# Performance work log

Hardware: AMD Instinct MI355X
Metric: run time of the kernel (lower is better)

Reference implementation:

```python
import jax, jax.numpy as jnp
import numpy as np

NUM_HEADS = 16
HEAD_DIM = 64  # hidden_size 1024 / 16 heads


def setup_inputs() -> dict:
    key = jax.random.key(0)
    ks = jax.random.split(key, 5)
    B, S, D = 4, 2048, 1024
    std = 0.02
    return {
        "hidden_states": jax.random.normal(ks[0], (B, S, D), jnp.float32),
        "attention_mask": jnp.zeros((B, 1, 1, S), jnp.float32),
        "Wq": jax.random.normal(ks[1], (D, D), jnp.float32) * std,
        "bq": jnp.zeros((D,), jnp.float32),
        "Wk": jax.random.normal(ks[2], (D, D), jnp.float32) * std,
        "bk": jnp.zeros((D,), jnp.float32),
        "Wv": jax.random.normal(ks[3], (D, D), jnp.float32) * std,
        "bv": jnp.zeros((D,), jnp.float32),
    }


def _split_heads(x):
    # [B, S, H*dh] -> [B, H, S, dh]
    B, S, _ = x.shape
    return x.reshape(B, S, NUM_HEADS, HEAD_DIM).transpose(0, 2, 1, 3)


def reference(hidden_states, attention_mask, Wq, bq, Wk, bk, Wv, bv):
    q = _split_heads(hidden_states @ Wq + bq)  # [B,H,S,dh]
    k = _split_heads(hidden_states @ Wk + bk)
    v = _split_heads(hidden_states @ Wv + bv)
    scale = 1.0 / jnp.sqrt(jnp.asarray(HEAD_DIM, q.dtype))
    scores = jnp.einsum("bhqd,bhkd->bhqk", q, k) * scale
    scores = scores + attention_mask.astype(scores.dtype)
    probs = jax.nn.softmax(scores, axis=-1)  # dropout prob = 0 -> identity
    ctx = jnp.einsum("bhqk,bhkd->bhqd", probs, v)
    B, H, S, dh = ctx.shape
    return ctx.transpose(0, 2, 1, 3).reshape(B, S, H * dh)
```

## Files before the change

### kernel.cpp

```cpp
#include <hip/hip_runtime.h>
#include <stdint.h>

typedef unsigned short u16;
typedef __attribute__((ext_vector_type(4))) float f32x4;
typedef __attribute__((ext_vector_type(8))) short bf16x8;
typedef __attribute__((ext_vector_type(4))) int i32x4;

#define LOG2E 1.4426950408889634f

__device__ inline u16 f2b(float x) {
  union { float f; uint32_t u; } t; t.f = x;
  uint32_t r = t.u + 0x7FFFu + ((t.u >> 16) & 1u);
  return (u16)(r >> 16);
}

__device__ inline int cvtpk(float a, float b) {
  int r;
  asm("v_cvt_pk_bf16_f32 %0, %1, %2" : "=v"(r) : "v"(a), "v"(b));
  return r;
}

__device__ inline float exp2a(float x) {
  float r;
  asm("v_exp_f32 %0, %1" : "=v"(r) : "v"(x));
  return r;
}

typedef const __attribute__((address_space(1))) void* gas_t;
typedef __attribute__((address_space(3))) void* las_t;
__device__ inline void gld16(const void* g, void* l) {
  __builtin_amdgcn_global_load_lds((gas_t)g, (las_t)l, 16, 0, 0);
}

__global__ void cvt_hs_k(const float* __restrict__ in, u16* __restrict__ outp, int n) {
  int i = (blockIdx.x * 256 + threadIdx.x) * 4;
  if (i >= n) return;
  float4 v = *(const float4*)(in + i);
  ushort4 o = { f2b(v.x), f2b(v.y), f2b(v.z), f2b(v.w) };
  *(ushort4*)(outp + i) = o;
}

__global__ void twk(const float* __restrict__ Wq, const float* __restrict__ Wk,
                    const float* __restrict__ Wv, u16* __restrict__ Wt) {
  __shared__ float tile[64][65];
  const float* W = (blockIdx.z == 0) ? Wq : ((blockIdx.z == 1) ? Wk : Wv);
  int n0 = blockIdx.x * 64, k0 = blockIdx.y * 64;
  int tid = threadIdx.x;
#pragma unroll 4
  for (int i = 0; i < 16; ++i) {
    int idx = i * 256 + tid; int r = idx >> 6, c = idx & 63;
    tile[r][c] = W[(k0 + r) * 1024 + n0 + c];
  }
  __syncthreads();
  u16* dst = Wt + blockIdx.z * 1048576;
#pragma unroll 4
  for (int i = 0; i < 16; ++i) {
    int idx = i * 256 + tid; int r = idx >> 6, c = idx & 63;
    dst[(n0 + r) * 1024 + k0 + c] = f2b(tile[c][r]);
  }
}

__global__ __launch_bounds__(256) void qkv_gemm_k(
    const u16* __restrict__ hsb, const u16* __restrict__ wt,
    const float* __restrict__ bq, const float* __restrict__ bk, const float* __restrict__ bv,
    u16* __restrict__ Qo, u16* __restrict__ Ko, u16* __restrict__ Vto) {
  __shared__ u16 t1[128 * 64];
  __shared__ u16 t2[128 * 64];
  const int tid = threadIdx.x;
  const int w = tid >> 6, l = tid & 63, g = l >> 4, lm = l & 15;

  int lin = blockIdx.y * 24 + blockIdx.x;
  lin = (lin & 7) * 192 + (lin >> 3);
  const int bx = lin % 24, by = lin / 24;

  const int nbase = bx * 128;
  const int wi = nbase >> 10;
  const int nloc0 = nbase & 1023;
  const int mbase = by * 128;
  const bool swapped = (wi < 2);
  const u16* T1g = swapped ? (wt + wi * 1048576 + nloc0 * 1024) : (hsb + mbase * 1024);
  const u16* T2g = swapped ? (hsb + mbase * 1024) : (wt + 2 * 1048576 + nloc0 * 1024);

  f32x4 acc[4][4];
#pragma unroll
  for (int i = 0; i < 4; ++i)
#pragma unroll
    for (int j = 0; j < 4; ++j)
#pragma unroll
      for (int r = 0; r < 4; ++r) acc[i][j][r] = 0.f;

  const int r1w = (w >> 1) * 64;
  const int r2w = (w & 1) * 64;

  for (int kb = 0; kb < 1024; kb += 64) {
    __syncthreads();
#pragma unroll
    for (int p = 0; p < 4; ++p) {
      int idx = p * 256 + tid;
      int r = idx >> 3, c = idx & 7;
      int sc = (c ^ (r & 7)) << 3;
      gld16(T1g + r * 1024 + kb + sc, t1 + idx * 8);
      gld16(T2g + r * 1024 + kb + sc, t2 + idx * 8);
    }
    __syncthreads();
#pragma unroll
    for (int ks = 0; ks < 2; ++ks) {
      bf16x8 fa[4], fb[4];
#pragma unroll
      for (int i = 0; i < 4; ++i) {
        int ra = r1w + i * 16 + lm;
        fa[i] = *(const bf16x8*)(t1 + ra * 64 + (((g + 4 * ks) ^ (ra & 7)) << 3));
        int rb = r2w + i * 16 + lm;
        fb[i] = *(const bf16x8*)(t2 + rb * 64 + (((g + 4 * ks) ^ (rb & 7)) << 3));
      }
      __builtin_amdgcn_s_setprio(1);
#pragma unroll
      for (int i = 0; i < 4; ++i)
#pragma unroll
        for (int j = 0; j < 4; ++j)
          acc[i][j] = __builtin_amdgcn_mfma_f32_16x16x32_bf16(fa[i], fb[j], acc[i][j], 0, 0, 0);
      __builtin_amdgcn_s_setprio(0);
    }
  }

  if (swapped) {
    u16* O = (wi == 0) ? Qo : Ko;
    const float* bias = (wi == 0) ? bq : bk;
#pragma unroll
    for (int i = 0; i < 4; ++i) {
      int nl = nloc0 + r1w + i * 16 + g * 4;
      f32x4 bv4 = *(const f32x4*)(bias + nl);
      int d = nl & 63, h = nl >> 6;
#pragma unroll
      for (int j = 0; j < 4; ++j) {
        int m = mbase + r2w + j * 16 + lm;
        int bb = m >> 11, s = m & 2047;
        f32x4 v = acc[i][j];
        ushort4 o = { f2b(v[0] + bv4[0]), f2b(v[1] + bv4[1]),
                      f2b(v[2] + bv4[2]), f2b(v[3] + bv4[3]) };
        *(ushort4*)(O + ((size_t)(bb * 16 + h) * 2048 + s) * 64 + d) = o;
      }
    }
  } else {
#pragma unroll
    for (int j = 0; j < 4; ++j) {
      int nl = nloc0 + r2w + j * 16 + lm;
      float bias = bv[nl];
      int d = nl & 63, h = nl >> 6;
#pragma unroll
      for (int i = 0; i < 4; ++i) {
        int m = mbase + r1w + i * 16 + g * 4;
        int bb = m >> 11, s = m & 2047;
        int cp = (s & ~31) | (((s >> 2) & 3) << 3) | (((s >> 4) & 1) << 2);
        f32x4 v = acc[i][j];
        ushort4 o = { f2b(v[0] + bias), f2b(v[1] + bias),
                      f2b(v[2] + bias), f2b(v[3] + bias) };
        *(ushort4*)(Vto + ((size_t)(bb * 16 + h) * 64 + d) * 2048 + cp) = o;
      }
    }
  }
}

__global__ __launch_bounds__(512) void attn_k(
    const u16* __restrict__ Qg, const u16* __restrict__ Kg, const u16* __restrict__ Vtg,
    const float* __restrict__ maskg, float* __restrict__ outp) {
  __shared__ u16 kt[128 * 64];
  __shared__ u16 vt[64 * 128];
  __shared__ float mk[128];
  const int tid = threadIdx.x;
  const int w = tid >> 6, l = tid & 63, g = l >> 4, lm = l & 15;

  int bid = blockIdx.y * 16 + blockIdx.x;
  bid = (bid & 7) * 128 + (bid >> 3);
  const int bx = bid & 15, bh = bid >> 4;
  const int b = bh >> 4, h = bh & 15;
  const int q0 = bx * 128 + w * 16;
  const u16* Qb = Qg + ((size_t)bh * 2048 + q0) * 64;
  const u16* Kb = Kg + (size_t)bh * 2048 * 64;
  const u16* Vb = Vtg + (size_t)bh * 64 * 2048;
  const float* mb = maskg + b * 2048;

  bf16x8 qf0 = *(const bf16x8*)(Qb + lm * 64 + g * 8);
  bf16x8 qf1 = *(const bf16x8*)(Qb + lm * 64 + 32 + g * 8);

  f32x4 ctx[4];
#pragma unroll
  for (int dt = 0; dt < 4; ++dt)
#pragma unroll
    for (int r = 0; r < 4; ++r) ctx[dt][r] = 0.f;
  float mrun = -3.0e38f, lrun = 0.f;
  const float QS = 0.125f * LOG2E;

  for (int kv = 0; kv < 2048; kv += 128) {
    __syncthreads();
#pragma unroll
    for (int p = 0; p < 2; ++p) {
      int idx = p * 512 + tid;
      int rk = idx >> 3, ck = idx & 7;
      gld16(Kb + (size_t)(kv + rk) * 64 + ((ck ^ (rk & 7)) << 3), kt + idx * 8);
      int rv = idx >> 4, cv = idx & 15;
      gld16(Vb + (size_t)rv * 2048 + kv + ((cv ^ (rv & 7)) << 3), vt + idx * 8);
    }
    if (tid < 128) mk[tid] = mb[kv + tid] * LOG2E;
    __syncthreads();

    f32x4 st[8];
#pragma unroll
    for (int t = 0; t < 8; ++t)
#pragma unroll
      for (int r = 0; r < 4; ++r) st[t][r] = 0.f;

    __builtin_amdgcn_s_setprio(1);
#pragma unroll
    for (int ks = 0; ks < 2; ++ks) {
      bf16x8 qf = ks ? qf1 : qf0;
#pragma unroll
      for (int t = 0; t < 8; ++t) {
        int r = t * 16 + lm;
        bf16x8 kf = *(const bf16x8*)(kt + r * 64 + (((g + 4 * ks) ^ (r & 7)) << 3));
        st[t] = __builtin_amdgcn_mfma_f32_16x16x32_bf16(kf, qf, st[t], 0, 0, 0);
      }
    }
    __builtin_amdgcn_s_setprio(0);

    float tmax = -3.0e38f;
#pragma unroll
    for (int t = 0; t < 8; ++t) {
      f32x4 mv = *(const f32x4*)(mk + t * 16 + g * 4);
#pragma unroll
      for (int r = 0; r < 4; ++r) st[t][r] = fmaf(st[t][r], QS, mv[r]);
      tmax = fmaxf(tmax, fmaxf(fmaxf(st[t][0], st[t][1]), fmaxf(st[t][2], st[t][3])));
    }
    tmax = fmaxf(tmax, __shfl_xor(tmax, 16));
    tmax = fmaxf(tmax, __shfl_xor(tmax, 32));

    if (!__all(tmax <= mrun + 8.0f)) {
      float mnew = fmaxf(mrun, tmax);
      float corr = exp2a(mrun - mnew);
      lrun *= corr;
#pragma unroll
      for (int dt = 0; dt < 4; ++dt)
#pragma unroll
        for (int r = 0; r < 4; ++r) ctx[dt][r] *= corr;
      mrun = mnew;
    }

    int pt[8][2];
    float lsum = 0.f;
#pragma unroll
    for (int t = 0; t < 8; ++t) {
      float p0 = exp2a(st[t][0] - mrun);
      float p1 = exp2a(st[t][1] - mrun);
      float p2 = exp2a(st[t][2] - mrun);
      float p3 = exp2a(st[t][3] - mrun);
      lsum += (p0 + p1) + (p2 + p3);
      pt[t][0] = cvtpk(p0, p1);
      pt[t][1] = cvtpk(p2, p3);
    }
    lsum += __shfl_xor(lsum, 16);
    lsum += __shfl_xor(lsum, 32);
    lrun += lsum;

    __builtin_amdgcn_s_setprio(1);
#pragma unroll
    for (int tp = 0; tp < 4; ++tp) {
      i32x4 pbi = { pt[2 * tp][0], pt[2 * tp][1], pt[2 * tp + 1][0], pt[2 * tp + 1][1] };
      bf16x8 pb = __builtin_bit_cast(bf16x8, pbi);
#pragma unroll
      for (int dt = 0; dt < 4; ++dt) {
        int r = dt * 16 + lm;
        bf16x8 va = *(const bf16x8*)(vt + r * 128 + (((tp * 4 + g) ^ (r & 7)) << 3));
        ctx[dt] = __builtin_amdgcn_mfma_f32_16x16x32_bf16(va, pb, ctx[dt], 0, 0, 0);
      }
    }
    __builtin_amdgcn_s_setprio(0);
  }

  float inv = 1.f / lrun;
  int sq = q0 + lm;
  float* ob = outp + ((size_t)(b * 2048 + sq)) * 1024 + h * 64;
#pragma unroll
  for (int dt = 0; dt < 4; ++dt) {
    f32x4 o;
#pragma unroll
    for (int r = 0; r < 4; ++r) o[r] = ctx[dt][r] * inv;
    *(f32x4*)(ob + dt * 16 + g * 4) = o;
  }
}

extern "C" void kernel_launch(void* const* d_in, const int* in_sizes, int n_in,
                              void* d_out, int out_size, void* d_ws, size_t ws_size,
                              hipStream_t stream) {
  const float* hs   = (const float*)d_in[0];
  const float* mask = (const float*)d_in[1];
  const float* Wq   = (const float*)d_in[2];
  const float* bq   = (const float*)d_in[3];
  const float* Wk   = (const float*)d_in[4];
  const float* bk   = (const float*)d_in[5];
  const float* Wv   = (const float*)d_in[6];
  const float* bv   = (const float*)d_in[7];
  float* out = (float*)d_out;

  char* ws = (char*)d_ws;
  u16* hsb = (u16*)(ws);
  u16* wt  = (u16*)(ws + (16u << 20));
  u16* Qb  = (u16*)(ws + (24u << 20));
  u16* Kb  = (u16*)(ws + (40u << 20));
  u16* Vtb = (u16*)(ws + (56u << 20));

  cvt_hs_k<<<dim3(8192), dim3(256), 0, stream>>>(hs, hsb, 8388608);
  twk<<<dim3(16, 16, 3), dim3(256), 0, stream>>>(Wq, Wk, Wv, wt);
  qkv_gemm_k<<<dim3(24, 64), dim3(256), 0, stream>>>(hsb, wt, bq, bk, bv, Qb, Kb, Vtb);
  attn_k<<<dim3(16, 64), dim3(512), 0, stream>>>(Qb, Kb, Vtb, mask, out);
}
```

Baseline: 267.6 us.

## Double-buffer LDS tiles in QKV GEMM and attention, enlarge GEMM tiles

The QKV GEMM moves to 256x256 tiles with 512 threads and double-buffered LDS, prefetching the next K slice while MFMAs run on the current one. The attention kernel also double-buffers its K/V tiles, preloads the whole mask row into LDS once, and uses a single vmcnt-wait barrier per iteration instead of two syncthreads. The aim is to hide global-load latency and cut barrier overhead. The cost is much higher LDS use (128KB in the GEMM, about 72KB in attention) and more register pressure, which may reduce occupancy.

```diff
diff --git a/kernel.cpp b/kernel.cpp
--- a/kernel.cpp
+++ b/kernel.cpp
@@ -30,6 +30,13 @@
 typedef __attribute__((address_space(3))) void* las_t;
 __device__ inline void gld16(const void* g, void* l) {
   __builtin_amdgcn_global_load_lds((gas_t)g, (las_t)l, 16, 0, 0);
+}
+
+__device__ inline void vm0_bar() {
+  asm volatile("s_waitcnt vmcnt(0)" ::: "memory");
+  __builtin_amdgcn_sched_barrier(0);
+  __builtin_amdgcn_s_barrier();
+  __builtin_amdgcn_sched_barrier(0);
 }
 
 __global__ void cvt_hs_k(const float* __restrict__ in, u16* __restrict__ outp, int n) {
@@ -60,101 +67,134 @@
   }
 }
 
-__global__ __launch_bounds__(256) void qkv_gemm_k(
+__global__ __launch_bounds__(512, 2) void qkv_gemm_k(
     const u16* __restrict__ hsb, const u16* __restrict__ wt,
     const float* __restrict__ bq, const float* __restrict__ bk, const float* __restrict__ bv,
     u16* __restrict__ Qo, u16* __restrict__ Ko, u16* __restrict__ Vto) {
-  __shared__ u16 t1[128 * 64];
-  __shared__ u16 t2[128 * 64];
+  __shared__ u16 lh[2][256 * 64];
+  __shared__ u16 lw[2][256 * 64];
   const int tid = threadIdx.x;
   const int w = tid >> 6, l = tid & 63, g = l >> 4, lm = l & 15;
-
-  int lin = blockIdx.y * 24 + blockIdx.x;
-  lin = (lin & 7) * 192 + (lin >> 3);
-  const int bx = lin % 24, by = lin / 24;
-
-  const int nbase = bx * 128;
+  const int wm = w >> 2, wn = w & 3;
+
+  int lin = blockIdx.y * 12 + blockIdx.x;
+  lin = (lin & 7) * 48 + (lin >> 3);
+  const int bx = lin % 12, by = lin / 12;
+  const int nbase = bx << 8;
   const int wi = nbase >> 10;
   const int nloc0 = nbase & 1023;
-  const int mbase = by * 128;
-  const bool swapped = (wi < 2);
-  const u16* T1g = swapped ? (wt + wi * 1048576 + nloc0 * 1024) : (hsb + mbase * 1024);
-  const u16* T2g = swapped ? (hsb + mbase * 1024) : (wt + 2 * 1048576 + nloc0 * 1024);
-
-  f32x4 acc[4][4];
-#pragma unroll
-  for (int i = 0; i < 4; ++i)
+  const int mbase = by << 8;
+  const u16* hsg = hsb + (size_t)mbase * 1024;
+  const u16* wg  = wt + (size_t)wi * 1048576 + (size_t)nloc0 * 1024;
+
+  f32x4 acc[8][4];
+#pragma unroll
+  for (int i = 0; i < 8; ++i)
 #pragma unroll
     for (int j = 0; j < 4; ++j)
 #pragma unroll
       for (int r = 0; r < 4; ++r) acc[i][j][r] = 0.f;
 
-  const int r1w = (w >> 1) * 64;
-  const int r2w = (w & 1) * 64;
-
-  for (int kb = 0; kb < 1024; kb += 64) {
-    __syncthreads();
-#pragma unroll
-    for (int p = 0; p < 4; ++p) {
-      int idx = p * 256 + tid;
-      int r = idx >> 3, c = idx & 7;
-      int sc = (c ^ (r & 7)) << 3;
-      gld16(T1g + r * 1024 + kb + sc, t1 + idx * 8);
-      gld16(T2g + r * 1024 + kb + sc, t2 + idx * 8);
-    }
-    __syncthreads();
-#pragma unroll
-    for (int ks = 0; ks < 2; ++ks) {
-      bf16x8 fa[4], fb[4];
-#pragma unroll
-      for (int i = 0; i < 4; ++i) {
-        int ra = r1w + i * 16 + lm;
-        fa[i] = *(const bf16x8*)(t1 + ra * 64 + (((g + 4 * ks) ^ (ra & 7)) << 3));
-        int rb = r2w + i * 16 + lm;
-        fb[i] = *(const bf16x8*)(t2 + rb * 64 + (((g + 4 * ks) ^ (rb & 7)) << 3));
+#pragma unroll
+  for (int p = 0; p < 4; ++p) {
+    int idx = p * 512 + tid;
+    int r = idx >> 3, c8 = idx & 7;
+    int sc = (c8 ^ (r & 7)) << 3;
+    gld16(hsg + (size_t)r * 1024 + sc, &lh[0][idx * 8]);
+    gld16(wg + (size_t)r * 1024 + sc, &lw[0][idx * 8]);
+  }
+  vm0_bar();
+
+  for (int t = 0; t < 16; ++t) {
+    const int cur = t & 1;
+    if (t < 15) {
+      const int kb = (t + 1) << 6;
+#pragma unroll
+      for (int p = 0; p < 4; ++p) {
+        int idx = p * 512 + tid;
+        int r = idx >> 3, c8 = idx & 7;
+        int sc = (c8 ^ (r & 7)) << 3;
+        gld16(hsg + (size_t)r * 1024 + kb + sc, &lh[cur ^ 1][idx * 8]);
+        gld16(wg + (size_t)r * 1024 + kb + sc, &lw[cur ^ 1][idx * 8]);
+      }
+    }
+    const u16* LH = lh[cur];
+    const u16* LW = lw[cur];
+    bf16x8 fw[4][2];
+#pragma unroll
+    for (int ni = 0; ni < 4; ++ni) {
+      int rb = wn * 64 + ni * 16 + lm;
+#pragma unroll
+      for (int ks = 0; ks < 2; ++ks)
+        fw[ni][ks] = *(const bf16x8*)(LW + rb * 64 + (((g + 4 * ks) ^ (rb & 7)) << 3));
+    }
+#pragma unroll
+    for (int mh = 0; mh < 2; ++mh) {
+      bf16x8 fh[4][2];
+#pragma unroll
+      for (int mi = 0; mi < 4; ++mi) {
+        int ra = wm * 128 + mh * 64 + mi * 16 + lm;
+#pragma unroll
+        for (int ks = 0; ks < 2; ++ks)
+          fh[mi][ks] = *(const bf16x8*)(LH + ra * 64 + (((g + 4 * ks) ^ (ra & 7)) << 3));
       }
       __builtin_amdgcn_s_setprio(1);
-#pragma unroll
-      for (int i = 0; i < 4; ++i)
-#pragma unroll
-        for (int j = 0; j < 4; ++j)
-          acc[i][j] = __builtin_amdgcn_mfma_f32_16x16x32_bf16(fa[i], fb[j], acc[i][j], 0, 0, 0);
+      if (wi < 2) {
+#pragma unroll
+        for (int mi = 0; mi < 4; ++mi)
+#pragma unroll
+          for (int ni = 0; ni < 4; ++ni)
+#pragma unroll
+            for (int ks = 0; ks < 2; ++ks)
+              acc[mh * 4 + mi][ni] = __builtin_amdgcn_mfma_f32_16x16x32_bf16(
+                  fw[ni][ks], fh[mi][ks], acc[mh * 4 + mi][ni], 0, 0, 0);
+      } else {
+#pragma unroll
+        for (int mi = 0; mi < 4; ++mi)
+#pragma unroll
+          for (int ni = 0; ni < 4; ++ni)
+#pragma unroll
+            for (int ks = 0; ks < 2; ++ks)
+              acc[mh * 4 + mi][ni] = __builtin_amdgcn_mfma_f32_16x16x32_bf16(
+                  fh[mi][ks], fw[ni][ks], acc[mh * 4 + mi][ni], 0, 0, 0);
+      }
       __builtin_amdgcn_s_setprio(0);
     }
-  }
-
-  if (swapped) {
+    vm0_bar();
+  }
+
+  if (wi < 2) {
     u16* O = (wi == 0) ? Qo : Ko;
     const float* bias = (wi == 0) ? bq : bk;
 #pragma unroll
-    for (int i = 0; i < 4; ++i) {
-      int nl = nloc0 + r1w + i * 16 + g * 4;
-      f32x4 bv4 = *(const f32x4*)(bias + nl);
+    for (int ni = 0; ni < 4; ++ni) {
+      int nl = nloc0 + wn * 64 + ni * 16 + g * 4;
+      f32x4 b4 = *(const f32x4*)(bias + nl);
       int d = nl & 63, h = nl >> 6;
 #pragma unroll
-      for (int j = 0; j < 4; ++j) {
-        int m = mbase + r2w + j * 16 + lm;
+      for (int mi = 0; mi < 8; ++mi) {
+        int m = mbase + wm * 128 + mi * 16 + lm;
         int bb = m >> 11, s = m & 2047;
-        f32x4 v = acc[i][j];
-        ushort4 o = { f2b(v[0] + bv4[0]), f2b(v[1] + bv4[1]),
-                      f2b(v[2] + bv4[2]), f2b(v[3] + bv4[3]) };
+        f32x4 v = acc[mi][ni];
+        ushort4 o = { f2b(v[0] + b4[0]), f2b(v[1] + b4[1]),
+                      f2b(v[2] + b4[2]), f2b(v[3] + b4[3]) };
         *(ushort4*)(O + ((size_t)(bb * 16 + h) * 2048 + s) * 64 + d) = o;
       }
     }
   } else {
 #pragma unroll
-    for (int j = 0; j < 4; ++j) {
-      int nl = nloc0 + r2w + j * 16 + lm;
-      float bias = bv[nl];
+    for (int ni = 0; ni < 4; ++ni) {
+      int nl = nloc0 + wn * 64 + ni * 16 + lm;
+      float bsc = bv[nl];
       int d = nl & 63, h = nl >> 6;
 #pragma unroll
-      for (int i = 0; i < 4; ++i) {
-        int m = mbase + r1w + i * 16 + g * 4;
+      for (int mi = 0; mi < 8; ++mi) {
+        int m = mbase + wm * 128 + mi * 16 + g * 4;
         int bb = m >> 11, s = m & 2047;
         int cp = (s & ~31) | (((s >> 2) & 3) << 3) | (((s >> 4) & 1) << 2);
-        f32x4 v = acc[i][j];
-        ushort4 o = { f2b(v[0] + bias), f2b(v[1] + bias),
-                      f2b(v[2] + bias), f2b(v[3] + bias) };
+        f32x4 v = acc[mi][ni];
+        ushort4 o = { f2b(v[0] + bsc), f2b(v[1] + bsc),
+                      f2b(v[2] + bsc), f2b(v[3] + bsc) };
         *(ushort4*)(Vto + ((size_t)(bb * 16 + h) * 64 + d) * 2048 + cp) = o;
       }
     }
@@ -164,9 +204,9 @@
 __global__ __launch_bounds__(512) void attn_k(
     const u16* __restrict__ Qg, const u16* __restrict__ Kg, const u16* __restrict__ Vtg,
     const float* __restrict__ maskg, float* __restrict__ outp) {
-  __shared__ u16 kt[128 * 64];
-  __shared__ u16 vt[64 * 128];
-  __shared__ float mk[128];
+  __shared__ u16 kts[2][128 * 64];
+  __shared__ u16 vts[2][64 * 128];
+  __shared__ float ml[2048];
   const int tid = threadIdx.x;
   const int w = tid >> 6, l = tid & 63, g = l >> 4, lm = l & 15;
 
@@ -191,45 +231,65 @@
   float mrun = -3.0e38f, lrun = 0.f;
   const float QS = 0.125f * LOG2E;
 
-  for (int kv = 0; kv < 2048; kv += 128) {
-    __syncthreads();
-#pragma unroll
-    for (int p = 0; p < 2; ++p) {
-      int idx = p * 512 + tid;
-      int rk = idx >> 3, ck = idx & 7;
-      gld16(Kb + (size_t)(kv + rk) * 64 + ((ck ^ (rk & 7)) << 3), kt + idx * 8);
-      int rv = idx >> 4, cv = idx & 15;
-      gld16(Vb + (size_t)rv * 2048 + kv + ((cv ^ (rv & 7)) << 3), vt + idx * 8);
-    }
-    if (tid < 128) mk[tid] = mb[kv + tid] * LOG2E;
-    __syncthreads();
+  {
+    f32x4 mv = *(const f32x4*)(mb + tid * 4);
+    *(f32x4*)(ml + tid * 4) = mv * LOG2E;
+  }
+#pragma unroll
+  for (int p = 0; p < 2; ++p) {
+    int idx = p * 512 + tid;
+    int rk = idx >> 3, ck = idx & 7;
+    gld16(Kb + (size_t)rk * 64 + ((ck ^ (rk & 7)) << 3), &kts[0][idx * 8]);
+    int rv = idx >> 4, cv = idx & 15;
+    gld16(Vb + (size_t)rv * 2048 + ((cv ^ (rv & 7)) << 3), &vts[0][idx * 8]);
+  }
+  asm volatile("s_waitcnt vmcnt(0) lgkmcnt(0)" ::: "memory");
+  __builtin_amdgcn_sched_barrier(0);
+  __builtin_amdgcn_s_barrier();
+  __builtin_amdgcn_sched_barrier(0);
+
+  for (int t = 0; t < 16; ++t) {
+    const int kv = t << 7, cur = t & 1;
+    if (t < 15) {
+      const int kv2 = kv + 128;
+#pragma unroll
+      for (int p = 0; p < 2; ++p) {
+        int idx = p * 512 + tid;
+        int rk = idx >> 3, ck = idx & 7;
+        gld16(Kb + (size_t)(kv2 + rk) * 64 + ((ck ^ (rk & 7)) << 3), &kts[cur ^ 1][idx * 8]);
+        int rv = idx >> 4, cv = idx & 15;
+        gld16(Vb + (size_t)rv * 2048 + kv2 + ((cv ^ (rv & 7)) << 3), &vts[cur ^ 1][idx * 8]);
+      }
+    }
+    const u16* kt = kts[cur];
+    const u16* vt = vts[cur];
 
     f32x4 st[8];
 #pragma unroll
-    for (int t = 0; t < 8; ++t)
-#pragma unroll
-      for (int r = 0; r < 4; ++r) st[t][r] = 0.f;
+    for (int t8 = 0; t8 < 8; ++t8)
+#pragma unroll
+      for (int r = 0; r < 4; ++r) st[t8][r] = 0.f;
 
     __builtin_amdgcn_s_setprio(1);
 #pragma unroll
     for (int ks = 0; ks < 2; ++ks) {
       bf16x8 qf = ks ? qf1 : qf0;
 #pragma unroll
-      for (int t = 0; t < 8; ++t) {
-        int r = t * 16 + lm;
+      for (int t8 = 0; t8 < 8; ++t8) {
+        int r = t8 * 16 + lm;
         bf16x8 kf = *(const bf16x8*)(kt + r * 64 + (((g + 4 * ks) ^ (r & 7)) << 3));
-        st[t] = __builtin_amdgcn_mfma_f32_16x16x32_bf16(kf, qf, st[t], 0, 0, 0);
+        st[t8] = __builtin_amdgcn_mfma_f32_16x16x32_bf16(kf, qf, st[t8], 0, 0, 0);
       }
     }
     __builtin_amdgcn_s_setprio(0);
 
     float tmax = -3.0e38f;
 #pragma unroll
-    for (int t = 0; t < 8; ++t) {
-      f32x4 mv = *(const f32x4*)(mk + t * 16 + g * 4);
-#pragma unroll
-      for (int r = 0; r < 4; ++r) st[t][r] = fmaf(st[t][r], QS, mv[r]);
-      tmax = fmaxf(tmax, fmaxf(fmaxf(st[t][0], st[t][1]), fmaxf(st[t][2], st[t][3])));
+    for (int t8 = 0; t8 < 8; ++t8) {
+      f32x4 mv = *(const f32x4*)(ml + kv + t8 * 16 + g * 4);
+#pragma unroll
+      for (int r = 0; r < 4; ++r) st[t8][r] = fmaf(st[t8][r], QS, mv[r]);
+      tmax = fmaxf(fmaxf(fmaxf(fmaxf(st[t8][0], st[t8][1]), st[t8][2]), st[t8][3]), tmax);
     }
     tmax = fmaxf(tmax, __shfl_xor(tmax, 16));
     tmax = fmaxf(tmax, __shfl_xor(tmax, 32));
@@ -248,14 +308,14 @@
     int pt[8][2];
     float lsum = 0.f;
 #pragma unroll
-    for (int t = 0; t < 8; ++t) {
-      float p0 = exp2a(st[t][0] - mrun);
-      float p1 = exp2a(st[t][1] - mrun);
-      float p2 = exp2a(st[t][2] - mrun);
-      float p3 = exp2a(st[t][3] - mrun);
+    for (int t8 = 0; t8 < 8; ++t8) {
+      float p0 = exp2a(st[t8][0] - mrun);
+      float p1 = exp2a(st[t8][1] - mrun);
+      float p2 = exp2a(st[t8][2] - mrun);
+      float p3 = exp2a(st[t8][3] - mrun);
       lsum += (p0 + p1) + (p2 + p3);
-      pt[t][0] = cvtpk(p0, p1);
-      pt[t][1] = cvtpk(p2, p3);
+      pt[t8][0] = cvtpk(p0, p1);
+      pt[t8][1] = cvtpk(p2, p3);
     }
     lsum += __shfl_xor(lsum, 16);
     lsum += __shfl_xor(lsum, 32);
@@ -274,6 +334,8 @@
       }
     }
     __builtin_amdgcn_s_setprio(0);
+
+    vm0_bar();
   }
 
   float inv = 1.f / lrun;
@@ -310,6 +372,6 @@
 
   cvt_hs_k<<<dim3(8192), dim3(256), 0, stream>>>(hs, hsb, 8388608);
   twk<<<dim3(16, 16, 3), dim3(256), 0, stream>>>(Wq, Wk, Wv, wt);
-  qkv_gemm_k<<<dim3(24, 64), dim3(256), 0, stream>>>(hsb, wt, bq, bk, bv, Qb, Kb, Vtb);
+  qkv_gemm_k<<<dim3(12, 32), dim3(512), 0, stream>>>(hsb, wt, bq, bk, bv, Qb, Kb, Vtb);
   attn_k<<<dim3(16, 64), dim3(512), 0, stream>>>(Qb, Kb, Vtb, mask, out);
 }
```

Result: slower. 346.2 us (+29.4%).
